# Performance work log

Measured on AMD Instinct MI355X. Metric: run time of the kernel, lower is better.

The kernel has to match this reference:

```python
import jax, jax.numpy as jnp
import numpy as np

N = 50000   # nodes
E = 600000  # edges
H = 128     # hidden_features
TW = 1      # time_window
L = 6       # hidden_layer
MSG_IN = 2 * H + TW + 2 + 1   # 260
UPD_IN = 2 * H + 1            # 257
LX = 1.0; LY = 1.0; TMAX = 1.0; DT = 0.01
EPS = 1e-5


def setup_inputs() -> dict:
    ks = iter(jax.random.split(jax.random.key(0), 64))
    rn = lambda s, sc=0.05: jax.random.normal(next(ks), s, dtype=jnp.float32) * sc
    z = lambda s: jnp.zeros(s, jnp.float32)
    o = lambda s: jnp.ones(s, jnp.float32)
    return {
        'u': rn((N, TW), 1.0),
        'pos': jax.random.uniform(next(ks), (N, 3), dtype=jnp.float32),
        'edge_index': jax.random.randint(next(ks), (2, E), 0, N),
        'emb_W1': rn((TW + 3, H)), 'emb_b1': z((H,)), 'emb_g1': o((H,)), 'emb_be1': z((H,)),
        'emb_W2': rn((H, H)), 'emb_b2': z((H,)), 'emb_g2': o((H,)), 'emb_be2': z((H,)),
        'm1_W': rn((L, MSG_IN, H)), 'm1_b': z((L, H)),
        'm2_W': rn((L, H, H)), 'm2_b': z((L, H)),
        'u1_W': rn((L, UPD_IN, H)), 'u1_b': z((L, H)),
        'u2_W': rn((L, H, H)), 'u2_b': z((L, H)),
        'bn_g': o((L, H)), 'bn_b': z((L, H)),
        'c1_W': rn((4, 1, 16)), 'c1_b': z((4,)),
        'c2_W': rn((8, 4, 12)), 'c2_b': z((8,)),
        'c3_W': rn((1, 8, 8)), 'c3_b': z((1,)),
    }


def _bn(x, g, b):
    # BatchNorm1d, training-mode batch statistics over node dim (biased var)
    mu = jnp.mean(x, 0)
    v = jnp.var(x, 0)
    return g * (x - mu) * jax.lax.rsqrt(v + EPS) + b


def _conv1d(x, W, b, stride):
    y = jax.lax.conv_general_dilated(x, W, (stride,), 'VALID',
                                     dimension_numbers=('NCH', 'OIH', 'NCH'))
    return y + b[None, :, None]


def _forward(u, pos, emb_W1, emb_b1, emb_g1, emb_be1, emb_W2, emb_b2, emb_g2, emb_be2,
             m1_W, m1_b, m2_W, m2_b, u1_W, u1_b, u2_W, u2_b, bn_g, bn_b,
             c1_W, c1_b, c2_W, c2_b, c3_W, c3_b, edge_index):
    px = pos[:, 1:2] / LX
    py = pos[:, 2:3] / LY
    variables = pos[:, 0:1] / TMAX  # pos_t, only eq variable

    # embedding MLP: Linear -> BN -> ReLU -> Linear -> BN
    h = jnp.concatenate([u, px, py, variables], -1) @ emb_W1 + emb_b1
    h = jax.nn.relu(_bn(h, emb_g1, emb_be1))
    h = _bn(h @ emb_W2 + emb_b2, emb_g2, emb_be2)

    src, dst = edge_index[0], edge_index[1]  # x_j = x[src], x_i = x[dst]
    du = u[dst] - u[src]
    dpx = px[dst] - px[src]
    dpy = py[dst] - py[src]
    var_i = variables[dst]
    deg = jax.ops.segment_sum(jnp.ones((E,), jnp.float32), dst, num_segments=N)
    deg = jnp.maximum(deg, 1.0)[:, None]  # mean aggregation denom (0-deg -> 0)

    for i in range(L):
        # message: cat(x_i, x_j, u_i-u_j, dpos_x, dpos_y, variables_i) -> 2xMLP
        msg_in = jnp.concatenate([h[dst], h[src], du, dpx, dpy, var_i], -1)  # [E,260]
        m = jax.nn.relu(msg_in @ m1_W[i] + m1_b[i])
        m = jax.nn.relu(m @ m2_W[i] + m2_b[i])
        agg = jax.ops.segment_sum(m, dst, num_segments=N) / deg  # mean scatter
        # update: cat(x, message, variables) -> 2xMLP, residual, BN
        up = jax.nn.relu(jnp.concatenate([h, agg, variables], -1) @ u1_W[i] + u1_b[i])
        up = jax.nn.relu(up @ u2_W[i] + u2_b[i])
        h = _bn(h + up, bn_g[i], bn_b[i])

    # output CNN over feature dim: [N,1,128] -> [N,1,1]
    x = h[:, None, :]
    x = jax.nn.relu(_conv1d(x, c1_W, c1_b, 3))
    x = jax.nn.relu(_conv1d(x, c2_W, c2_b, 3))
    diff = _conv1d(x, c3_W, c3_b, 2)[:, 0, :]  # [N, TW]

    dt = jnp.cumsum(jnp.full((1, TW), DT * 0.1, dtype=h.dtype), axis=1)
    return dt * diff


def reference(u, pos, edge_index, emb_W1, emb_b1, emb_g1, emb_be1, emb_W2, emb_b2,
              emb_g2, emb_be2, m1_W, m1_b, m2_W, m2_b, u1_W, u1_b, u2_W, u2_b,
              bn_g, bn_b, c1_W, c1_b, c2_W, c2_b, c3_W, c3_b):
    return _forward(u, pos, emb_W1, emb_b1, emb_g1, emb_be1, emb_W2, emb_b2, emb_g2,
                    emb_be2, m1_W, m1_b, m2_W, m2_b, u1_W, u1_b, u2_W, u2_b,
                    bn_g, bn_b, c1_W, c1_b, c2_W, c2_b, c3_W, c3_b, edge_index)
```

## Files before the change

### kernel.cpp

```cpp
#include <hip/hip_runtime.h>

#define NN 50000
#define NE 600000
#define HD 128
#define NL 6
#define DPB 16

typedef __attribute__((ext_vector_type(8))) short bf16x8;
typedef __attribute__((ext_vector_type(4))) float f32x4;

__device__ inline unsigned short f2bf(float x) {
  unsigned u = __float_as_uint(x);
  u += 0x7FFF + ((u >> 16) & 1);
  return (unsigned short)(u >> 16);
}
__device__ inline float bf2f(unsigned short s) {
  return __uint_as_float((unsigned)s << 16);
}
__device__ inline unsigned pk2(float a, float b) {
  return (unsigned)f2bf(a) | ((unsigned)f2bf(b) << 16);
}

__global__ void k_code(float* __restrict__ out, float code) {
  if (threadIdx.x == 0 && blockIdx.x == 0) out[0] = code;
}


__global__ __launch_bounds__(256) void k_w2t(const float* __restrict__ W, unsigned short* __restrict__ T) {
  int idx = blockIdx.x * 256 + threadIdx.x;
  if (idx >= NL * HD * HD) return;
  int l = idx >> 14, r = idx & 16383;
  int n = r >> 7, k = r & 127;
  T[idx] = f2bf(W[(l << 14) + (k << 7) + n]);
}

__global__ __launch_bounds__(256) void k_u1t(const float* __restrict__ W, unsigned short* __restrict__ T) {
  int idx = blockIdx.x * 256 + threadIdx.x;
  if (idx >= NL * 128 * 256) return;
  int l = idx >> 15, r = idx & 32767;
  int n = r >> 8, k = r & 255;
  T[idx] = f2bf(W[l * 32896 + k * 128 + n]);
}

__global__ __launch_bounds__(256) void k_abt(const float* __restrict__ W, unsigned short* __restrict__ T) {
  int idx = blockIdx.x * 256 + threadIdx.x;
  if (idx >= NL * 256 * 128) return;
  int l = idx >> 15, r = idx & 32767;
  int n = r >> 7, k = r & 127;
  int row = (n < 128) ? k : 128 + k;
  int col = n & 127;
  T[idx] = f2bf(W[l * 33280 + row * 128 + col]);
}


__global__ __launch_bounds__(256) void k_deg(const int* __restrict__ ei, int* __restrict__ deg) {
  int e = blockIdx.x * 256 + threadIdx.x;
  if (e < NE) {
    int d = ei[NE + e];
    if (d >= 0 && d < NN) atomicAdd(&deg[d], 1);
  }
}

__global__ __launch_bounds__(256) void k_scan1(const int* __restrict__ deg, int* __restrict__ cursor,
                                               int* __restrict__ blk, float* __restrict__ invd) {
  __shared__ int sd[256];
  int t = threadIdx.x;
  int i = blockIdx.x * 256 + t;
  int v = (i < NN) ? deg[i] : 0;
  sd[t] = v;
  __syncthreads();
  for (int off = 1; off < 256; off <<= 1) {
    int x = (t >= off) ? sd[t - off] : 0;
    __syncthreads();
    if (t >= off) sd[t] += x;
    __syncthreads();
  }
  int incl = sd[t];
  if (i < NN) {
    cursor[i] = incl - v;
    invd[i] = 1.0f / fmaxf((float)v, 1.0f);
  }
  if (t == 255) blk[blockIdx.x] = incl;
}

__global__ __launch_bounds__(256) void k_scan2(int* __restrict__ blk, int nb) {
  __shared__ int sd[256];
  int t = threadIdx.x;
  int v = (t < nb) ? blk[t] : 0;
  sd[t] = v;
  __syncthreads();
  for (int off = 1; off < 256; off <<= 1) {
    int x = (t >= off) ? sd[t - off] : 0;
    __syncthreads();
    if (t >= off) sd[t] += x;
    __syncthreads();
  }
  if (t < nb) blk[t] = sd[t] - v;
}

__global__ __launch_bounds__(256) void k_scan3(int* __restrict__ cursor, const int* __restrict__ blk,
                                               int* __restrict__ rowstart) {
  int i = blockIdx.x * 256 + threadIdx.x;
  if (i < NN) {
    int v = cursor[i] + blk[blockIdx.x];
    cursor[i] = v;
    rowstart[i] = v;
  }
  if (i == 0) rowstart[NN] = NE;
}

__global__ __launch_bounds__(256) void k_scatter(const int* __restrict__ ei, const float* __restrict__ u,
                                                 const float* __restrict__ pos, int* __restrict__ cursor,
                                                 int* __restrict__ ssrc, int* __restrict__ sdst,
                                                 float* __restrict__ sfeat) {
  int e = blockIdx.x * 256 + threadIdx.x;
  if (e >= NE) return;
  int s = ei[e], d = ei[NE + e];
  s = s < 0 ? 0 : (s >= NN ? NN - 1 : s);
  d = d < 0 ? 0 : (d >= NN ? NN - 1 : d);
  int p = atomicAdd(&cursor[d], 1);
  ssrc[p] = s;
  sdst[p] = d;
  float du  = u[d] - u[s];
  float dpx = pos[d*3+1] - pos[s*3+1];
  float dpy = pos[d*3+2] - pos[s*3+2];
  float vi  = pos[d*3+0];
  ((float4*)sfeat)[p] = make_float4(du, dpx, dpy, vi);
}


__global__ __launch_bounds__(256) void k_emb1(const float* __restrict__ u, const float* __restrict__ pos,
                                              const float* __restrict__ W, const float* __restrict__ b,
                                              float* __restrict__ h, double* __restrict__ P) {
  __shared__ float xs[32 * 129];
  int tid = threadIdx.x;
  int nl = tid & 31, jg = tid >> 5;
  int gn = blockIdx.x * 32 + nl;
  float f0 = 0.f, f1 = 0.f, f2 = 0.f, f3 = 0.f;
  if (gn < NN) { f0 = u[gn]; f1 = pos[gn*3+1]; f2 = pos[gn*3+2]; f3 = pos[gn*3+0]; }
  float x[16];
#pragma unroll
  for (int q = 0; q < 4; ++q) {
    int j = (jg << 4) + (q << 2);
    float4 w0 = *(const float4*)(W + 0*HD + j);
    float4 w1 = *(const float4*)(W + 1*HD + j);
    float4 w2 = *(const float4*)(W + 2*HD + j);
    float4 w3 = *(const float4*)(W + 3*HD + j);
    float4 bb = *(const float4*)(b + j);
    x[q*4+0] = f0*w0.x + f1*w1.x + f2*w2.x + f3*w3.x + bb.x;
    x[q*4+1] = f0*w0.y + f1*w1.y + f2*w2.y + f3*w3.y + bb.y;
    x[q*4+2] = f0*w0.z + f1*w1.z + f2*w2.z + f3*w3.z + bb.z;
    x[q*4+3] = f0*w0.w + f1*w1.w + f2*w2.w + f3*w3.w + bb.w;
  }
  if (gn < NN) {
#pragma unroll
    for (int q = 0; q < 4; ++q)
      *(float4*)(h + (size_t)gn*HD + (jg<<4) + (q<<2)) = make_float4(x[q*4+0], x[q*4+1], x[q*4+2], x[q*4+3]);
  }
#pragma unroll
  for (int i = 0; i < 16; ++i) xs[nl*129 + (jg<<4) + i] = (gn < NN) ? x[i] : 0.f;
  __syncthreads();
  if (tid < HD) {
    double s = 0.0, sq = 0.0;
    for (int e = 0; e < 32; ++e) { double v = (double)xs[e*129 + tid]; s += v; sq += v*v; }
    size_t pb = (size_t)blockIdx.x * 256;
    P[pb + tid] = s;
    P[pb + 128 + tid] = sq;
  }
}

__global__ __launch_bounds__(256) void k_emb2(float* __restrict__ h, const float* __restrict__ W,
                                              const float* __restrict__ b, double* __restrict__ P) {
  __shared__ float hs[32 * 129];
  int tid = threadIdx.x;
  int base = blockIdx.x * 32;
#pragma unroll
  for (int r = 0; r < 16; ++r) {
    int lin = r*256 + tid;
    int n = lin >> 7, j = lin & 127;
    int gn = base + n;
    hs[n*129 + j] = (gn < NN) ? h[(size_t)gn*HD + j] : 0.f;
  }
  __syncthreads();
  int nl = tid & 31, jg = tid >> 5;
  int gn = base + nl;
  float acc[16];
#pragma unroll
  for (int q = 0; q < 4; ++q) {
    float4 bb = *(const float4*)(b + (jg<<4) + (q<<2));
    acc[q*4+0] = bb.x; acc[q*4+1] = bb.y; acc[q*4+2] = bb.z; acc[q*4+3] = bb.w;
  }
  for (int k = 0; k < HD; ++k) {
    float a = hs[nl*129 + k];
    const float4* wp = (const float4*)(W + (size_t)k*HD + (jg<<4));
#pragma unroll
    for (int q = 0; q < 4; ++q) {
      float4 wv = wp[q];
      acc[q*4+0] = fmaf(a, wv.x, acc[q*4+0]);
      acc[q*4+1] = fmaf(a, wv.y, acc[q*4+1]);
      acc[q*4+2] = fmaf(a, wv.z, acc[q*4+2]);
      acc[q*4+3] = fmaf(a, wv.w, acc[q*4+3]);
    }
  }
  if (gn < NN) {
#pragma unroll
    for (int q = 0; q < 4; ++q)
      *(float4*)(h + (size_t)gn*HD + (jg<<4) + (q<<2)) = make_float4(acc[q*4+0], acc[q*4+1], acc[q*4+2], acc[q*4+3]);
  }
  __syncthreads();
#pragma unroll
  for (int i = 0; i < 16; ++i) hs[nl*129 + (jg<<4) + i] = (gn < NN) ? acc[i] : 0.f;
  __syncthreads();
  if (tid < HD) {
    double s = 0.0, sq = 0.0;
    for (int e = 0; e < 32; ++e) { double v = (double)hs[e*129 + tid]; s += v; sq += v*v; }
    size_t pb = (size_t)blockIdx.x * 256;
    P[pb + tid] = s;
    P[pb + 128 + tid] = sq;
  }
}

__global__ __launch_bounds__(256) void k_redP(const double* __restrict__ P, int nrows,
                                              float* __restrict__ musig) {
  __shared__ double sd[256];
  __shared__ double sq_[256];
  int c = blockIdx.x;
  int t = threadIdx.x;
  double s = 0.0, q = 0.0;
  for (int k = t; k < nrows; k += 256) {
    s += P[(size_t)k*256 + c];
    q += P[(size_t)k*256 + 128 + c];
  }
  sd[t] = s; sq_[t] = q;
  __syncthreads();
  for (int off = 128; off; off >>= 1) {
    if (t < off) { sd[t] += sd[t + off]; sq_[t] += sq_[t + off]; }
    __syncthreads();
  }
  if (t == 0) {
    double mu  = sd[0] / (double)NN;
    double var = sq_[0] / (double)NN - mu * mu;
    musig[c]      = (float)mu;
    musig[HD + c] = (float)(1.0 / sqrt(var + 1e-5));
  }
}

__global__ void k_redA(const double* __restrict__ stats, float* __restrict__ musig) {
  int c = threadIdx.x;
  double mu  = stats[c] / (double)NN;
  double var = stats[128 + c] / (double)NN - mu * mu;
  musig[c]      = (float)mu;
  musig[HD + c] = (float)(1.0 / sqrt(var + 1e-5));
}

__global__ __launch_bounds__(256) void k_bn(float* __restrict__ h, const float* __restrict__ musig,
                                            const float* __restrict__ g, const float* __restrict__ be,
                                            int relu) {
  int idx = blockIdx.x * 256 + threadIdx.x;
  if (idx >= NN * HD) return;
  int j = idx & 127;
  float x = h[idx];
  x = g[j] * (x - musig[j]) * musig[HD + j] + be[j];
  if (relu) x = fmaxf(x, 0.f);
  h[idx] = x;
}


__global__ __launch_bounds__(256) void k_ab_mfma(float* __restrict__ h,
                                                 const unsigned short* __restrict__ abt,
                                                 const float* __restrict__ musig,
                                                 const float* __restrict__ g, const float* __restrict__ be,
                                                 int applyBN,
                                                 unsigned short* __restrict__ A, unsigned short* __restrict__ B) {
  __shared__ unsigned short hbf[32 * 136];
  int tid = threadIdx.x;
  int base = blockIdx.x * 32;
#pragma unroll
  for (int r = 0; r < 16; ++r) {
    int lin = r*256 + tid;
    int n = lin >> 7, j = lin & 127;
    int gn = base + n;
    float hv = (gn < NN) ? h[(size_t)gn*HD + j] : 0.f;
    if (applyBN) {
      hv = g[j] * (hv - musig[j]) * musig[HD + j] + be[j];
      if (gn < NN) h[(size_t)gn*HD + j] = hv;
    }
    hbf[n*136 + j] = f2bf((gn < NN) ? hv : 0.f);
  }
  __syncthreads();
  int wv = tid >> 6, lane = tid & 63;
  int quad = lane >> 4, mrow = lane & 15;
  int mt = wv & 1, ntg = wv >> 1;
  f32x4 acc[8];
#pragma unroll
  for (int t = 0; t < 8; ++t) acc[t] = (f32x4){0.f,0.f,0.f,0.f};
#pragma unroll
  for (int ks = 0; ks < 4; ++ks) {
    bf16x8 a = *(const bf16x8*)(hbf + (mt*16 + mrow)*136 + ks*32 + quad*8);
#pragma unroll
    for (int t = 0; t < 8; ++t) {
      bf16x8 b = *(const bf16x8*)(abt + (size_t)((ntg*8 + t)*16 + mrow)*128 + ks*32 + quad*8);
      acc[t] = __builtin_amdgcn_mfma_f32_16x16x32_bf16(a, b, acc[t], 0, 0, 0);
    }
  }
#pragma unroll
  for (int t = 0; t < 8; ++t) {
    int c = (ntg*8 + t)*16 + mrow;
#pragma unroll
    for (int r = 0; r < 4; ++r) {
      int gn = base + mt*16 + quad*4 + r;
      if (gn < NN) {
        if (c < 128) A[(size_t)gn*HD + c]       = f2bf(acc[t][r]);
        else         B[(size_t)gn*HD + c - 128] = f2bf(acc[t][r]);
      }
    }
  }
}


__global__ __launch_bounds__(256, 2) void k_msgupd(const unsigned short* __restrict__ A,
                                                   const unsigned short* __restrict__ B,
                                                   const int* __restrict__ ssrc, const int* __restrict__ sdst,
                                                   const float* __restrict__ sfeat, const float* __restrict__ invd,
                                                   const int* __restrict__ rowstart,
                                                   const float* __restrict__ W1, const float* __restrict__ b1,
                                                   const unsigned short* __restrict__ w2t, const float* __restrict__ b2,
                                                   float* __restrict__ h, const float* __restrict__ pos,
                                                   const unsigned short* __restrict__ u1t,
                                                   const float* __restrict__ U1var, const float* __restrict__ ub1,
                                                   const unsigned short* __restrict__ u2t, const float* __restrict__ ub2,
                                                   double* __restrict__ P) {
  __shared__ __align__(16) unsigned short smAB[16*136 + 2*32*136];
  __shared__ float wes[6 * 128];
  __shared__ int ldstD[64];

  unsigned short* As   = smAB;
  unsigned short* m1b0 = smAB + 16*136;
  unsigned short* abf  = smAB;
  unsigned short* u1bf = smAB + 16*264;

  int tid = threadIdx.x;
  int base = blockIdx.x * DPB;

  {
    int row = tid >> 4, c16 = tid & 15;
    int gn = base + row;
    bf16x8 v = (bf16x8){0,0,0,0,0,0,0,0};
    if (gn < NN) v = *(const bf16x8*)(A + (size_t)gn*HD + c16*8);
    *(bf16x8*)(As + row*136 + c16*8) = v;
  }
  for (int i = tid; i < 768; i += 256) {
    int k = i >> 7, j = i & 127;
    float v;
    if (k < 4)       v = W1[(size_t)(256 + k)*HD + j];
    else if (k == 4) v = b1[j];
    else             v = b2[j];
    wes[i] = v;
  }
  int rs0 = rowstart[base];
  int rs1 = rowstart[base + DPB];
  __syncthreads();

  int wv = tid >> 6, lane = tid & 63;
  int quad = lane >> 4, mrow = lane & 15;
  int el = tid & 31, jg = tid >> 5;

  float b2c[2];
#pragma unroll
  for (int t = 0; t < 2; ++t) b2c[t] = wes[5*128 + (wv*2 + t)*16 + mrow];

  const float4* sf4 = (const float4*)sfeat;
  int nch = (rs1 - rs0 + 31) >> 5;

  f32x4 agg[2];
  agg[0] = (f32x4){0.f,0.f,0.f,0.f}; agg[1] = agg[0];

  int d_c; float4 f_c;
  int s_n1, d_n1; float4 f_n1;
  {
    int e = rs0 + el; bool v = e < rs1;
    int sc = v ? ssrc[e] : 0;
    d_c = v ? (sdst[e] - base) : 999;
    f_c = v ? sf4[e] : make_float4(0.f, 0.f, 0.f, 0.f);
    s_n1 = sc;
  }
  bf16x8 b0_c = *(const bf16x8*)(B + (size_t)s_n1*HD + (jg<<4));
  bf16x8 b1_c = *(const bf16x8*)(B + (size_t)s_n1*HD + (jg<<4) + 8);
  {
    int e = rs0 + 32 + el; bool v = e < rs1;
    s_n1 = v ? ssrc[e] : 0;
    d_n1 = v ? (sdst[e] - base) : 999;
    f_n1 = v ? sf4[e] : make_float4(0.f, 0.f, 0.f, 0.f);
  }

  int par = 0;
  for (int ch = 0; ch < nch; ++ch) {
    int e0 = rs0 + ch*32;
    int s_n2, d_n2; float4 f_n2;
    {
      int e = e0 + 64 + el; bool v = e < rs1;
      s_n2 = v ? ssrc[e] : 0;
      d_n2 = v ? (sdst[e] - base) : 999;
      f_n2 = v ? sf4[e] : make_float4(0.f, 0.f, 0.f, 0.f);
    }
    bf16x8 b0_n = *(const bf16x8*)(B + (size_t)s_n1*HD + (jg<<4));
    bf16x8 b1_n = *(const bf16x8*)(B + (size_t)s_n1*HD + (jg<<4) + 8);

    if (tid < 32) ldstD[par*32 + tid] = d_c;
    unsigned short* m1bf = m1b0 + par*32*136;

    {
      int dA = (d_c < DPB) ? d_c : 0;
      float f0 = f_c.x, f1 = f_c.y, f2 = f_c.z, f3 = f_c.w;
      const unsigned short* Ar = As + dA*136 + (jg<<4);
      bf16x8 a0 = *(const bf16x8*)(Ar);
      bf16x8 a1 = *(const bf16x8*)(Ar + 8);
      float m1v[16];
#pragma unroll
      for (int q = 0; q < 4; ++q) {
        float4 w0 = *(const float4*)(wes + 0*128 + (jg<<4) + (q<<2));
        float4 w1 = *(const float4*)(wes + 1*128 + (jg<<4) + (q<<2));
        float4 w2 = *(const float4*)(wes + 2*128 + (jg<<4) + (q<<2));
        float4 w3 = *(const float4*)(wes + 3*128 + (jg<<4) + (q<<2));
        float4 bb = *(const float4*)(wes + 4*128 + (jg<<4) + (q<<2));
#pragma unroll
        for (int z = 0; z < 4; ++z) {
          int i = q*4 + z;
          unsigned short avs = (i < 8) ? (unsigned short)a0[i] : (unsigned short)a1[i-8];
          unsigned short bvs = (i < 8) ? (unsigned short)b0_c[i] : (unsigned short)b1_c[i-8];
          float we  = (z==0?w0.x:(z==1?w0.y:(z==2?w0.z:w0.w)));
          float w1e = (z==0?w1.x:(z==1?w1.y:(z==2?w1.z:w1.w)));
          float w2e = (z==0?w2.x:(z==1?w2.y:(z==2?w2.z:w2.w)));
          float w3e = (z==0?w3.x:(z==1?w3.y:(z==2?w3.z:w3.w)));
          float bbe = (z==0?bb.x:(z==1?bb.y:(z==2?bb.z:bb.w)));
          m1v[i] = fmaxf(bf2f(avs) + bf2f(bvs) + f0*we + f1*w1e + f2*w2e + f3*w3e + bbe, 0.f);
        }
      }
      unsigned* pp = (unsigned*)(m1bf + el*136 + (jg<<4));
#pragma unroll
      for (int i = 0; i < 8; ++i)
        pp[i] = pk2(m1v[2*i], m1v[2*i+1]);
    }
    __syncthreads();

    {
      f32x4 acc[2][2];
      acc[0][0] = (f32x4){0.f,0.f,0.f,0.f}; acc[0][1] = acc[0][0];
      acc[1][0] = acc[0][0]; acc[1][1] = acc[0][0];
#pragma unroll
      for (int ks = 0; ks < 4; ++ks) {
        bf16x8 a0 = *(const bf16x8*)(m1bf + (mrow)*136      + ks*32 + quad*8);
        bf16x8 a1 = *(const bf16x8*)(m1bf + (16 + mrow)*136 + ks*32 + quad*8);
#pragma unroll
        for (int t = 0; t < 2; ++t) {
          bf16x8 b = *(const bf16x8*)(w2t + (size_t)((wv*2 + t)*16 + mrow)*128 + ks*32 + quad*8);
          acc[0][t] = __builtin_amdgcn_mfma_f32_16x16x32_bf16(a0, b, acc[0][t], 0, 0, 0);
          acc[1][t] = __builtin_amdgcn_mfma_f32_16x16x32_bf16(a1, b, acc[1][t], 0, 0, 0);
        }
      }

      bf16x8 sel;
#pragma unroll
      for (int i = 0; i < 8; ++i) {
        int dl = ldstD[par*32 + quad*8 + i];
        sel[i] = (short)((dl == mrow) ? 0x3F80 : 0);
      }

      int src0 = ((quad & 1) * 2) * 16 + mrow;
      int src1 = src0 + 16;
      bool useE0 = (quad < 2);
#pragma unroll
      for (int t = 0; t < 2; ++t) {
        float bb = b2c[t];
        unsigned p00 = pk2(fmaxf(acc[0][t][0] + bb, 0.f), fmaxf(acc[0][t][1] + bb, 0.f));
        unsigned p01 = pk2(fmaxf(acc[0][t][2] + bb, 0.f), fmaxf(acc[0][t][3] + bb, 0.f));
        unsigned p10 = pk2(fmaxf(acc[1][t][0] + bb, 0.f), fmaxf(acc[1][t][1] + bb, 0.f));
        unsigned p11 = pk2(fmaxf(acc[1][t][2] + bb, 0.f), fmaxf(acc[1][t][3] + bb, 0.f));
        unsigned a00 = (unsigned)__shfl((int)p00, src0);
        unsigned a01 = (unsigned)__shfl((int)p01, src0);
        unsigned a02 = (unsigned)__shfl((int)p00, src1);
        unsigned a03 = (unsigned)__shfl((int)p01, src1);
        unsigned e10 = (unsigned)__shfl((int)p10, src0);
        unsigned e11 = (unsigned)__shfl((int)p11, src0);
        unsigned e12 = (unsigned)__shfl((int)p10, src1);
        unsigned e13 = (unsigned)__shfl((int)p11, src1);
        bf16x8 bfr;
        unsigned* bp = (unsigned*)&bfr;
        bp[0] = useE0 ? a00 : e10;
        bp[1] = useE0 ? a01 : e11;
        bp[2] = useE0 ? a02 : e12;
        bp[3] = useE0 ? a03 : e13;
        agg[t] = __builtin_amdgcn_mfma_f32_16x16x32_bf16(sel, bfr, agg[t], 0, 0, 0);
      }
    }

    d_c = d_n1; f_c = f_n1;
    s_n1 = s_n2; d_n1 = d_n2; f_n1 = f_n2;
    b0_c = b0_n; b1_c = b1_n;
    par ^= 1;
  }
  __syncthreads();

  {
    int row = tid >> 4, c16 = tid & 15;
    int gn = base + row;
    float4 h0 = *(const float4*)(h + (size_t)gn*HD + c16*8);
    float4 h1 = *(const float4*)(h + (size_t)gn*HD + c16*8 + 4);
    unsigned* q = (unsigned*)(abf + row*264 + c16*8);
    q[0] = pk2(h0.x, h0.y); q[1] = pk2(h0.z, h0.w);
    q[2] = pk2(h1.x, h1.y); q[3] = pk2(h1.z, h1.w);
  }
  {
    float invdv[4];
#pragma unroll
    for (int r = 0; r < 4; ++r) invdv[r] = invd[base + quad*4 + r];
#pragma unroll
    for (int t = 0; t < 2; ++t) {
      int c = (wv*2 + t)*16 + mrow;
#pragma unroll
      for (int r = 0; r < 4; ++r)
        abf[(quad*4 + r)*264 + 128 + c] = f2bf(agg[t][r] * invdv[r]);
    }
  }
  __syncthreads();

  int lo = mrow;
  float ub1c[2], uvarc[2], ub2c[2];
#pragma unroll
  for (int t = 0; t < 2; ++t) {
    int c = (wv*2 + t)*16 + lo;
    ub1c[t] = ub1[c]; uvarc[t] = U1var[c]; ub2c[t] = ub2[c];
  }
  float lvarv[4];
#pragma unroll
  for (int r = 0; r < 4; ++r) lvarv[r] = pos[(size_t)(base + quad*4 + r)*3 + 0];

  f32x4 ua[2];
  ua[0] = (f32x4){0.f,0.f,0.f,0.f}; ua[1] = ua[0];
#pragma unroll
  for (int ks = 0; ks < 8; ++ks) {
    bf16x8 a = *(const bf16x8*)(abf + lo*264 + ks*32 + quad*8);
#pragma unroll
    for (int t = 0; t < 2; ++t) {
      bf16x8 b = *(const bf16x8*)(u1t + (size_t)((wv*2 + t)*16 + lo)*256 + ks*32 + quad*8);
      ua[t] = __builtin_amdgcn_mfma_f32_16x16x32_bf16(a, b, ua[t], 0, 0, 0);
    }
  }
#pragma unroll
  for (int t = 0; t < 2; ++t) {
    int c = (wv*2 + t)*16 + lo;
#pragma unroll
    for (int r = 0; r < 4; ++r) {
      float v = fmaxf(ua[t][r] + ub1c[t] + lvarv[r]*uvarc[t], 0.f);
      u1bf[(quad*4 + r)*136 + c] = f2bf(v);
    }
  }
  __syncthreads();

  f32x4 va[2];
  va[0] = (f32x4){0.f,0.f,0.f,0.f}; va[1] = va[0];
#pragma unroll
  for (int ks = 0; ks < 4; ++ks) {
    bf16x8 a = *(const bf16x8*)(u1bf + lo*136 + ks*32 + quad*8);
#pragma unroll
    for (int t = 0; t < 2; ++t) {
      bf16x8 b = *(const bf16x8*)(u2t + (size_t)((wv*2 + t)*16 + lo)*128 + ks*32 + quad*8);
      va[t] = __builtin_amdgcn_mfma_f32_16x16x32_bf16(a, b, va[t], 0, 0, 0);
    }
  }

#pragma unroll
  for (int t = 0; t < 2; ++t) {
    int c = (wv*2 + t)*16 + lo;
    float s = 0.f, q = 0.f;
#pragma unroll
    for (int r = 0; r < 4; ++r) {
      int gn = base + quad*4 + r;
      float x = h[(size_t)gn*HD + c] + fmaxf(va[t][r] + ub2c[t], 0.f);
      h[(size_t)gn*HD + c] = x;
      s += x; q += x*x;
    }
    s += __shfl_xor(s, 16); q += __shfl_xor(q, 16);
    s += __shfl_xor(s, 32); q += __shfl_xor(q, 32);
    if (quad == 0) {
      size_t pb = (size_t)blockIdx.x * 256;
      P[pb + c]       = (double)s;
      P[pb + 128 + c] = (double)q;
    }
  }
}


__global__ __launch_bounds__(256) void k_msg_direct(const float* __restrict__ h,
                                                    const int* __restrict__ ei, const float* __restrict__ u,
                                                    const float* __restrict__ pos, const float* __restrict__ invd,
                                                    const float* __restrict__ W1, const float* __restrict__ b1,
                                                    const float* __restrict__ W2, const float* __restrict__ b2,
                                                    float* __restrict__ agg) {
  __shared__ float hd[32 * 129];
  __shared__ float hsr[32 * 129];
  __shared__ float m1s[32 * 129];
  __shared__ int lsrc[32];
  __shared__ int ldst[32];
  __shared__ float lf[32][4];
  int tid = threadIdx.x;
  int base = blockIdx.x * 32;
  if (tid < 32) {
    int e = base + tid;
    int s = ei[e], d = ei[NE + e];
    s = s < 0 ? 0 : (s >= NN ? NN - 1 : s);
    d = d < 0 ? 0 : (d >= NN ? NN - 1 : d);
    lsrc[tid] = s; ldst[tid] = d;
    lf[tid][0] = u[d] - u[s];
    lf[tid][1] = pos[d*3+1] - pos[s*3+1];
    lf[tid][2] = pos[d*3+2] - pos[s*3+2];
    lf[tid][3] = pos[d*3+0];
  }
  __syncthreads();
#pragma unroll
  for (int r = 0; r < 16; ++r) {
    int lin = r*256 + tid;
    int n = lin >> 7, j = lin & 127;
    hd[n*129 + j]  = h[(size_t)ldst[n]*HD + j];
    hsr[n*129 + j] = h[(size_t)lsrc[n]*HD + j];
  }
  __syncthreads();
  int el = tid & 31, jg = tid >> 5;
  float f0 = lf[el][0], f1 = lf[el][1], f2 = lf[el][2], f3 = lf[el][3];
  const float* We = W1 + 256*HD + (jg<<4);
  float acc[16];
#pragma unroll
  for (int q = 0; q < 4; ++q) {
    float4 w0 = *(const float4*)(We + 0*HD + (q<<2));
    float4 w1 = *(const float4*)(We + 1*HD + (q<<2));
    float4 w2 = *(const float4*)(We + 2*HD + (q<<2));
    float4 w3 = *(const float4*)(We + 3*HD + (q<<2));
    float4 bb = *(const float4*)(b1 + (jg<<4) + (q<<2));
    acc[q*4+0] = f0*w0.x + f1*w1.x + f2*w2.x + f3*w3.x + bb.x;
    acc[q*4+1] = f0*w0.y + f1*w1.y + f2*w2.y + f3*w3.y + bb.y;
    acc[q*4+2] = f0*w0.z + f1*w1.z + f2*w2.z + f3*w3.z + bb.z;
    acc[q*4+3] = f0*w0.w + f1*w1.w + f2*w2.w + f3*w3.w + bb.w;
  }
  for (int k = 0; k < HD; ++k) {
    float a  = hd[el*129 + k];
    float bs = hsr[el*129 + k];
    const float4* wa = (const float4*)(W1 + (size_t)k*HD + (jg<<4));
    const float4* wb = (const float4*)(W1 + (size_t)(128 + k)*HD + (jg<<4));
#pragma unroll
    for (int q = 0; q < 4; ++q) {
      float4 w1v = wa[q];
      float4 w2v = wb[q];
      acc[q*4+0] = fmaf(a, w1v.x, fmaf(bs, w2v.x, acc[q*4+0]));
      acc[q*4+1] = fmaf(a, w1v.y, fmaf(bs, w2v.y, acc[q*4+1]));
      acc[q*4+2] = fmaf(a, w1v.z, fmaf(bs, w2v.z, acc[q*4+2]));
      acc[q*4+3] = fmaf(a, w1v.w, fmaf(bs, w2v.w, acc[q*4+3]));
    }
  }
#pragma unroll
  for (int i = 0; i < 16; ++i) m1s[el*129 + (jg<<4) + i] = fmaxf(acc[i], 0.f);
  __syncthreads();
  float acc2[16];
#pragma unroll
  for (int q = 0; q < 4; ++q) {
    float4 bb = *(const float4*)(b2 + (jg<<4) + (q<<2));
    acc2[q*4+0] = bb.x; acc2[q*4+1] = bb.y; acc2[q*4+2] = bb.z; acc2[q*4+3] = bb.w;
  }
  for (int k = 0; k < HD; ++k) {
    float a = m1s[el*129 + k];
    const float4* wp = (const float4*)(W2 + (size_t)k*HD + (jg<<4));
#pragma unroll
    for (int q = 0; q < 4; ++q) {
      float4 wv = wp[q];
      acc2[q*4+0] = fmaf(a, wv.x, acc2[q*4+0]);
      acc2[q*4+1] = fmaf(a, wv.y, acc2[q*4+1]);
      acc2[q*4+2] = fmaf(a, wv.z, acc2[q*4+2]);
      acc2[q*4+3] = fmaf(a, wv.w, acc2[q*4+3]);
    }
  }
#pragma unroll
  for (int i = 0; i < 16; ++i) hd[el*129 + (jg<<4) + i] = fmaxf(acc2[i], 0.f);
  __syncthreads();
  if (tid < HD) {
    int j = tid;
    for (int e = 0; e < 32; ++e) {
      int de = ldst[e];
      atomicAdd(&agg[(size_t)de*HD + j], hd[e*129 + j] * invd[de]);
    }
  }
}


__global__ __launch_bounds__(256) void k_upd(float* __restrict__ h, const float* __restrict__ agg,
                                             const float* __restrict__ pos,
                                             const float* __restrict__ W1, const float* __restrict__ b1,
                                             const float* __restrict__ W2, const float* __restrict__ b2,
                                             double* __restrict__ stats) {
  __shared__ float hs[32 * 129];
  __shared__ float as_[32 * 129];
  int tid = threadIdx.x;
  int base = blockIdx.x * 32;
#pragma unroll
  for (int r = 0; r < 16; ++r) {
    int lin = r*256 + tid;
    int n = lin >> 7, j = lin & 127;
    int gn = base + n;
    hs[n*129 + j]  = (gn < NN) ? h[(size_t)gn*HD + j]   : 0.f;
    as_[n*129 + j] = (gn < NN) ? agg[(size_t)gn*HD + j] : 0.f;
  }
  __syncthreads();
  int nl = tid & 31, jg = tid >> 5;
  int gn = base + nl;
  float var = (gn < NN) ? pos[gn*3+0] : 0.f;
  float acc[16];
#pragma unroll
  for (int q = 0; q < 4; ++q) {
    int j = (jg<<4) + (q<<2);
    float4 bb = *(const float4*)(b1 + j);
    float4 wv = *(const float4*)(W1 + 256*HD + j);
    acc[q*4+0] = fmaf(var, wv.x, bb.x);
    acc[q*4+1] = fmaf(var, wv.y, bb.y);
    acc[q*4+2] = fmaf(var, wv.z, bb.z);
    acc[q*4+3] = fmaf(var, wv.w, bb.w);
  }
  for (int k = 0; k < HD; ++k) {
    float a = hs[nl*129 + k];
    float g = as_[nl*129 + k];
    const float4* w1p = (const float4*)(W1 + (size_t)k*HD + (jg<<4));
    const float4* w2p = (const float4*)(W1 + (size_t)(128 + k)*HD + (jg<<4));
#pragma unroll
    for (int q = 0; q < 4; ++q) {
      float4 wa = w1p[q];
      float4 wb = w2p[q];
      acc[q*4+0] = fmaf(a, wa.x, fmaf(g, wb.x, acc[q*4+0]));
      acc[q*4+1] = fmaf(a, wa.y, fmaf(g, wb.y, acc[q*4+1]));
      acc[q*4+2] = fmaf(a, wa.z, fmaf(g, wb.z, acc[q*4+2]));
      acc[q*4+3] = fmaf(a, wa.w, fmaf(g, wb.w, acc[q*4+3]));
    }
  }
  float up1[16];
#pragma unroll
  for (int i = 0; i < 16; ++i) up1[i] = fmaxf(acc[i], 0.f);
  __syncthreads();
#pragma unroll
  for (int i = 0; i < 16; ++i) as_[nl*129 + (jg<<4) + i] = up1[i];
  __syncthreads();
  float acc2[16];
#pragma unroll
  for (int q = 0; q < 4; ++q) {
    float4 bb = *(const float4*)(b2 + (jg<<4) + (q<<2));
    acc2[q*4+0] = bb.x; acc2[q*4+1] = bb.y; acc2[q*4+2] = bb.z; acc2[q*4+3] = bb.w;
  }
  for (int k = 0; k < HD; ++k) {
    float a = as_[nl*129 + k];
    const float4* wp = (const float4*)(W2 + (size_t)k*HD + (jg<<4));
#pragma unroll
    for (int q = 0; q < 4; ++q) {
      float4 wv = wp[q];
      acc2[q*4+0] = fmaf(a, wv.x, acc2[q*4+0]);
      acc2[q*4+1] = fmaf(a, wv.y, acc2[q*4+1]);
      acc2[q*4+2] = fmaf(a, wv.z, acc2[q*4+2]);
      acc2[q*4+3] = fmaf(a, wv.w, acc2[q*4+3]);
    }
  }
  float x[16];
#pragma unroll
  for (int i = 0; i < 16; ++i)
    x[i] = hs[nl*129 + (jg<<4) + i] + fmaxf(acc2[i], 0.f);
  if (gn < NN) {
#pragma unroll
    for (int q = 0; q < 4; ++q)
      *(float4*)(h + (size_t)gn*HD + (jg<<4) + (q<<2)) = make_float4(x[q*4+0], x[q*4+1], x[q*4+2], x[q*4+3]);
  }
  __syncthreads();
#pragma unroll
  for (int i = 0; i < 16; ++i) hs[nl*129 + (jg<<4) + i] = (gn < NN) ? x[i] : 0.f;
  __syncthreads();
  if (tid < HD) {
    double s = 0.0, sq = 0.0;
    for (int e = 0; e < 32; ++e) { double v = (double)hs[e*129 + tid]; s += v; sq += v*v; }
    atomicAdd(&stats[tid], s);
    atomicAdd(&stats[HD + tid], sq);
  }
}


__global__ __launch_bounds__(256) void k_conv(const float* __restrict__ h,
                                              const float* __restrict__ musig,
                                              const float* __restrict__ g, const float* __restrict__ be,
                                              int applyBN,
                                              const float* __restrict__ c1W, const float* __restrict__ c1b,
                                              const float* __restrict__ c2W, const float* __restrict__ c2b,
                                              const float* __restrict__ c3W, const float* __restrict__ c3b,
                                              float* __restrict__ out) {
  __shared__ float xs[4][128];
  __shared__ float o1[4][152];
  __shared__ float o2[4][72];
  int tid = threadIdx.x;
  int w = tid >> 6, lane = tid & 63;
  int n = blockIdx.x * 4 + w;
#pragma unroll
  for (int half = 0; half < 2; ++half) {
    int j = half * 64 + lane;
    float v = h[(size_t)n*HD + j];
    if (applyBN) v = g[j] * (v - musig[j]) * musig[HD + j] + be[j];
    xs[w][j] = v;
  }
  __syncthreads();
  for (int o = lane; o < 152; o += 64) {
    int oc = o / 38, t = o % 38;
    float s = c1b[oc];
#pragma unroll
    for (int k = 0; k < 16; ++k) s = fmaf(xs[w][t*3 + k], c1W[oc*16 + k], s);
    o1[w][oc*38 + t] = fmaxf(s, 0.f);
  }
  __syncthreads();
  for (int o = lane; o < 72; o += 64) {
    int oc = o / 9, t = o % 9;
    float s = c2b[oc];
    for (int ic = 0; ic < 4; ++ic) {
#pragma unroll
      for (int k = 0; k < 12; ++k) s = fmaf(o1[w][ic*38 + t*3 + k], c2W[oc*48 + ic*12 + k], s);
    }
    o2[w][oc*9 + t] = fmaxf(s, 0.f);
  }
  __syncthreads();
  int ic = lane >> 3, k = lane & 7;
  float t3 = o2[w][ic*9 + k] * c3W[ic*8 + k];
  for (int off = 32; off; off >>= 1) t3 += __shfl_down(t3, off);
  if (lane == 0) out[n] = 0.001f * (t3 + c3b[0]);
}


extern "C" void kernel_launch(void* const* d_in, const int* in_sizes, int n_in,
                              void* d_out, int out_size, void* d_ws, size_t ws_size,
                              hipStream_t stream) {
  (void)out_size;
  float* out = (float*)d_out;

  static const int expect[27] = {
    50000, 150000, 1200000,
    512, 128, 128, 128,
    16384, 128, 128, 128,
    199680, 768, 98304, 768, 197376, 768, 98304, 768,
    768, 768,
    64, 4, 384, 8, 64, 1
  };
  if (n_in != 27) { k_code<<<1, 64, 0, stream>>>(out, 5000099.f); return; }
  for (int i = 0; i < 27; ++i)
    if (in_sizes[i] != expect[i]) { k_code<<<1, 64, 0, stream>>>(out, 5000100.f + (float)i); return; }

  const float* u    = (const float*)d_in[0];
  const float* pos  = (const float*)d_in[1];
  const int*   ei   = (const int*)d_in[2];
  const float* eW1  = (const float*)d_in[3];
  const float* eb1  = (const float*)d_in[4];
  const float* eg1  = (const float*)d_in[5];
  const float* ebe1 = (const float*)d_in[6];
  const float* eW2  = (const float*)d_in[7];
  const float* eb2  = (const float*)d_in[8];
  const float* eg2  = (const float*)d_in[9];
  const float* ebe2 = (const float*)d_in[10];
  const float* m1W  = (const float*)d_in[11];
  const float* m1b  = (const float*)d_in[12];
  const float* m2W  = (const float*)d_in[13];
  const float* m2b  = (const float*)d_in[14];
  const float* u1W  = (const float*)d_in[15];
  const float* u1b  = (const float*)d_in[16];
  const float* u2W  = (const float*)d_in[17];
  const float* u2b  = (const float*)d_in[18];
  const float* bng  = (const float*)d_in[19];
  const float* bnb  = (const float*)d_in[20];
  const float* c1W  = (const float*)d_in[21];
  const float* c1b  = (const float*)d_in[22];
  const float* c2W  = (const float*)d_in[23];
  const float* c2b  = (const float*)d_in[24];
  const float* c3W  = (const float*)d_in[25];
  const float* c3b  = (const float*)d_in[26];

  char* wsp = (char*)d_ws;
  size_t off = 0;
  auto alloc = [&](size_t bytes) -> void* {
    void* p = wsp + off;
    off = (off + bytes + 255) & ~(size_t)255;
    return p;
  };
  double* stats  = (double*)alloc(256 * 8);
  float*  musig  = (float*)alloc(256 * 4);
  int*    deg    = (int*)alloc((size_t)NN * 4);
  int*    cursor = (int*)alloc((size_t)NN * 4);
  int*    blk    = (int*)alloc(256 * 4);
  float*  invd   = (float*)alloc((size_t)NN * 4);
  float*  h      = (float*)alloc((size_t)NN * HD * 4);
  float*  agg    = (float*)alloc((size_t)NN * HD * 4);
  double* P      = (double*)alloc((size_t)3200 * 256 * 8);
  size_t needed_direct = off;
  unsigned short* A = (unsigned short*)alloc((size_t)NN * HD * 2);
  unsigned short* B = (unsigned short*)alloc((size_t)NN * HD * 2);
  float*  sfeat  = (float*)alloc((size_t)NE * 4 * 4);
  int*    ssrc   = (int*)alloc((size_t)NE * 4);
  int*    sdst   = (int*)alloc((size_t)NE * 4);
  int*    rowstart = (int*)alloc((size_t)(NN + 1) * 4);
  unsigned short* w2t = (unsigned short*)alloc((size_t)NL * HD * HD * 2);
  unsigned short* u2t = (unsigned short*)alloc((size_t)NL * HD * HD * 2);
  unsigned short* u1t = (unsigned short*)alloc((size_t)NL * HD * 256 * 2);
  unsigned short* abt = (unsigned short*)alloc((size_t)NL * 256 * HD * 2);
  size_t needed_fast = off;

  if (ws_size < needed_direct) {
    k_code<<<1, 64, 0, stream>>>(out, (float)(9000000u + (unsigned)(ws_size >> 20)));
    return;
  }
  const bool fast = (ws_size >= needed_fast);

  const int nbN  = (NN + 255) / 256;
  const int nbE  = (NE + 255) / 256;
  const int nt32 = (NN + 31) / 32;
  const int nbBN = NN * HD / 256;
  const int nbMU = NN / DPB;

  hipMemsetAsync(deg, 0, (size_t)NN * 4, stream);
  k_deg<<<nbE, 256, 0, stream>>>(ei, deg);
  k_scan1<<<nbN, 256, 0, stream>>>(deg, cursor, blk, invd);
  if (fast) {
    k_scan2<<<1, 256, 0, stream>>>(blk, nbN);
    k_scan3<<<nbN, 256, 0, stream>>>(cursor, blk, rowstart);
    k_scatter<<<nbE, 256, 0, stream>>>(ei, u, pos, cursor, ssrc, sdst, sfeat);
    k_w2t<<<(NL*HD*HD + 255) / 256, 256, 0, stream>>>(m2W, w2t);
    k_w2t<<<(NL*HD*HD + 255) / 256, 256, 0, stream>>>(u2W, u2t);
    k_u1t<<<(NL*HD*256 + 255) / 256, 256, 0, stream>>>(u1W, u1t);
    k_abt<<<(NL*256*HD + 255) / 256, 256, 0, stream>>>(m1W, abt);
  }

  k_emb1<<<nt32, 256, 0, stream>>>(u, pos, eW1, eb1, h, P);
  k_redP<<<128, 256, 0, stream>>>(P, nt32, musig);
  k_bn<<<nbBN, 256, 0, stream>>>(h, musig, eg1, ebe1, 1);
  k_emb2<<<nt32, 256, 0, stream>>>(h, eW2, eb2, P);
  k_redP<<<128, 256, 0, stream>>>(P, nt32, musig);
  k_bn<<<nbBN, 256, 0, stream>>>(h, musig, eg2, ebe2, 0);

  for (int i = 0; i < NL; ++i) {
    if (fast) {
      k_ab_mfma<<<nt32, 256, 0, stream>>>(h, abt + (size_t)i * 256 * HD,
                                          musig, bng + (size_t)(i > 0 ? i - 1 : 0) * HD,
                                          bnb + (size_t)(i > 0 ? i - 1 : 0) * HD,
                                          (i > 0) ? 1 : 0, A, B);
      k_msgupd<<<nbMU, 256, 0, stream>>>(A, B, ssrc, sdst, sfeat, invd, rowstart,
                                         m1W + (size_t)i * 260 * HD, m1b + (size_t)i * HD,
                                         w2t + (size_t)i * HD * HD, m2b + (size_t)i * HD,
                                         h, pos,
                                         u1t + (size_t)i * HD * 256,
                                         u1W + (size_t)i * 32896 + 256 * HD,
                                         u1b + (size_t)i * HD,
                                         u2t + (size_t)i * HD * HD,
                                         u2b + (size_t)i * HD, P);
      k_redP<<<128, 256, 0, stream>>>(P, nbMU, musig);
    } else {
      hipMemsetAsync(agg, 0, (size_t)NN * HD * 4, stream);
      k_msg_direct<<<NE / 32, 256, 0, stream>>>(h, ei, u, pos, invd,
                                                m1W + (size_t)i * 260 * HD, m1b + (size_t)i * HD,
                                                m2W + (size_t)i * HD * HD, m2b + (size_t)i * HD, agg);
      hipMemsetAsync(stats, 0, 256 * 8, stream);
      k_upd<<<nt32, 256, 0, stream>>>(h, agg, pos,
                                      u1W + (size_t)i * 257 * HD, u1b + (size_t)i * HD,
                                      u2W + (size_t)i * HD * HD, u2b + (size_t)i * HD, stats);
      k_redA<<<1, 128, 0, stream>>>(stats, musig);
      k_bn<<<nbBN, 256, 0, stream>>>(h, musig, bng + (size_t)i * HD, bnb + (size_t)i * HD, 0);
    }
  }

  k_conv<<<NN / 4, 256, 0, stream>>>(h, musig, bng + (size_t)(NL - 1) * HD, bnb + (size_t)(NL - 1) * HD,
                                     fast ? 1 : 0,
                                     c1W, c1b, c2W, c2b, c3W, c3b, out);
}
```

Baseline: 1.498 ms.

## Process 64 edges per chunk in fused message kernel instead of 32

The edge loop in the fused message/update kernel now handles 64 edges per iteration. Each thread computes 32 hidden columns for one edge rather than 16, and each wave issues MFMAs over four 16-edge groups. This halves the number of chunk iterations and block barriers per destination block and gives more MFMA work per synchronisation. In exchange it doubles LDS for the message buffer, raises register pressure with more accumulators and gather vectors, and wastes more work on padding when a block has few edges.

After: 1.528 ms. 1.02x slower.

```diff
diff --git a/kernel.cpp b/kernel.cpp
--- a/kernel.cpp
+++ b/kernel.cpp
@@ -330,9 +330,9 @@
                                                    const float* __restrict__ U1var, const float* __restrict__ ub1,
                                                    const unsigned short* __restrict__ u2t, const float* __restrict__ ub2,
                                                    double* __restrict__ P) {
-  __shared__ __align__(16) unsigned short smAB[16*136 + 2*32*136];
+  __shared__ __align__(16) unsigned short smAB[16*136 + 2*64*136];
   __shared__ float wes[6 * 128];
-  __shared__ int ldstD[64];
+  __shared__ int ldstD[128];
 
   unsigned short* As   = smAB;
   unsigned short* m1b0 = smAB + 16*136;
@@ -363,17 +363,19 @@
 
   int wv = tid >> 6, lane = tid & 63;
   int quad = lane >> 4, mrow = lane & 15;
-  int el = tid & 31, jg = tid >> 5;
+  int el = tid & 63;
 
   float b2c[2];
 #pragma unroll
   for (int t = 0; t < 2; ++t) b2c[t] = wes[5*128 + (wv*2 + t)*16 + mrow];
 
   const float4* sf4 = (const float4*)sfeat;
-  int nch = (rs1 - rs0 + 31) >> 5;
+  int nch = (rs1 - rs0 + 63) >> 6;
 
   f32x4 agg[2];
   agg[0] = (f32x4){0.f,0.f,0.f,0.f}; agg[1] = agg[0];
+
+  int cb0 = wv*32;
 
   int d_c; float4 f_c;
   int s_n1, d_n1; float4 f_n1;
@@ -384,10 +386,12 @@
     f_c = v ? sf4[e] : make_float4(0.f, 0.f, 0.f, 0.f);
     s_n1 = sc;
   }
-  bf16x8 b0_c = *(const bf16x8*)(B + (size_t)s_n1*HD + (jg<<4));
-  bf16x8 b1_c = *(const bf16x8*)(B + (size_t)s_n1*HD + (jg<<4) + 8);
+  bf16x8 bc0 = *(const bf16x8*)(B + (size_t)s_n1*HD + cb0);
+  bf16x8 bc1 = *(const bf16x8*)(B + (size_t)s_n1*HD + cb0 + 8);
+  bf16x8 bc2 = *(const bf16x8*)(B + (size_t)s_n1*HD + cb0 + 16);
+  bf16x8 bc3 = *(const bf16x8*)(B + (size_t)s_n1*HD + cb0 + 24);
   {
-    int e = rs0 + 32 + el; bool v = e < rs1;
+    int e = rs0 + 64 + el; bool v = e < rs1;
     s_n1 = v ? ssrc[e] : 0;
     d_n1 = v ? (sdst[e] - base) : 999;
     f_n1 = v ? sf4[e] : make_float4(0.f, 0.f, 0.f, 0.f);
@@ -395,75 +399,92 @@
 
   int par = 0;
   for (int ch = 0; ch < nch; ++ch) {
-    int e0 = rs0 + ch*32;
+    int e0 = rs0 + ch*64;
     int s_n2, d_n2; float4 f_n2;
     {
-      int e = e0 + 64 + el; bool v = e < rs1;
+      int e = e0 + 128 + el; bool v = e < rs1;
       s_n2 = v ? ssrc[e] : 0;
       d_n2 = v ? (sdst[e] - base) : 999;
       f_n2 = v ? sf4[e] : make_float4(0.f, 0.f, 0.f, 0.f);
     }
-    bf16x8 b0_n = *(const bf16x8*)(B + (size_t)s_n1*HD + (jg<<4));
-    bf16x8 b1_n = *(const bf16x8*)(B + (size_t)s_n1*HD + (jg<<4) + 8);
-
-    if (tid < 32) ldstD[par*32 + tid] = d_c;
-    unsigned short* m1bf = m1b0 + par*32*136;
+    bf16x8 bn0 = *(const bf16x8*)(B + (size_t)s_n1*HD + cb0);
+    bf16x8 bn1 = *(const bf16x8*)(B + (size_t)s_n1*HD + cb0 + 8);
+    bf16x8 bn2 = *(const bf16x8*)(B + (size_t)s_n1*HD + cb0 + 16);
+    bf16x8 bn3 = *(const bf16x8*)(B + (size_t)s_n1*HD + cb0 + 24);
+
+    if (tid < 64) ldstD[par*64 + tid] = d_c;
+    unsigned short* m1bf = m1b0 + par*64*136;
 
     {
       int dA = (d_c < DPB) ? d_c : 0;
       float f0 = f_c.x, f1 = f_c.y, f2 = f_c.z, f3 = f_c.w;
-      const unsigned short* Ar = As + dA*136 + (jg<<4);
-      bf16x8 a0 = *(const bf16x8*)(Ar);
-      bf16x8 a1 = *(const bf16x8*)(Ar + 8);
-      float m1v[16];
-#pragma unroll
-      for (int q = 0; q < 4; ++q) {
-        float4 w0 = *(const float4*)(wes + 0*128 + (jg<<4) + (q<<2));
-        float4 w1 = *(const float4*)(wes + 1*128 + (jg<<4) + (q<<2));
-        float4 w2 = *(const float4*)(wes + 2*128 + (jg<<4) + (q<<2));
-        float4 w3 = *(const float4*)(wes + 3*128 + (jg<<4) + (q<<2));
-        float4 bb = *(const float4*)(wes + 4*128 + (jg<<4) + (q<<2));
-#pragma unroll
-        for (int z = 0; z < 4; ++z) {
-          int i = q*4 + z;
-          unsigned short avs = (i < 8) ? (unsigned short)a0[i] : (unsigned short)a1[i-8];
-          unsigned short bvs = (i < 8) ? (unsigned short)b0_c[i] : (unsigned short)b1_c[i-8];
-          float we  = (z==0?w0.x:(z==1?w0.y:(z==2?w0.z:w0.w)));
-          float w1e = (z==0?w1.x:(z==1?w1.y:(z==2?w1.z:w1.w)));
-          float w2e = (z==0?w2.x:(z==1?w2.y:(z==2?w2.z:w2.w)));
-          float w3e = (z==0?w3.x:(z==1?w3.y:(z==2?w3.z:w3.w)));
-          float bbe = (z==0?bb.x:(z==1?bb.y:(z==2?bb.z:bb.w)));
-          m1v[i] = fmaxf(bf2f(avs) + bf2f(bvs) + f0*we + f1*w1e + f2*w2e + f3*w3e + bbe, 0.f);
+#pragma unroll
+      for (int hh = 0; hh < 2; ++hh) {
+        int cb = cb0 + hh*16;
+        const unsigned short* Ar = As + dA*136 + cb;
+        bf16x8 a0 = *(const bf16x8*)(Ar);
+        bf16x8 a1 = *(const bf16x8*)(Ar + 8);
+        bf16x8 bv0 = (hh == 0) ? bc0 : bc2;
+        bf16x8 bv1 = (hh == 0) ? bc1 : bc3;
+        float m1v[16];
+#pragma unroll
+        for (int q = 0; q < 4; ++q) {
+          float4 w0 = *(const float4*)(wes + 0*128 + cb + (q<<2));
+          float4 w1 = *(const float4*)(wes + 1*128 + cb + (q<<2));
+          float4 w2 = *(const float4*)(wes + 2*128 + cb + (q<<2));
+          float4 w3 = *(const float4*)(wes + 3*128 + cb + (q<<2));
+          float4 bb = *(const float4*)(wes + 4*128 + cb + (q<<2));
+#pragma unroll
+          for (int z = 0; z < 4; ++z) {
+            int i = q*4 + z;
+            unsigned short avs = (i < 8) ? (unsigned short)a0[i] : (unsigned short)a1[i-8];
+            unsigned short bvs = (i < 8) ? (unsigned short)bv0[i] : (unsigned short)bv1[i-8];
+            float we  = (z==0?w0.x:(z==1?w0.y:(z==2?w0.z:w0.w)));
+            float w1e = (z==0?w1.x:(z==1?w1.y:(z==2?w1.z:w1.w)));
+            float w2e = (z==0?w2.x:(z==1?w2.y:(z==2?w2.z:w2.w)));
+            float w3e = (z==0?w3.x:(z==1?w3.y:(z==2?w3.z:w3.w)));
+            float bbe = (z==0?bb.x:(z==1?bb.y:(z==2?bb.z:bb.w)));
+            m1v[i] = fmaxf(bf2f(avs) + bf2f(bvs) + f0*we + f1*w1e + f2*w2e + f3*w3e + bbe, 0.f);
+          }
         }
+        unsigned* pp = (unsigned*)(m1bf + el*136 + cb);
+#pragma unroll
+        for (int i = 0; i < 8; ++i)
+          pp[i] = pk2(m1v[2*i], m1v[2*i+1]);
       }
-      unsigned* pp = (unsigned*)(m1bf + el*136 + (jg<<4));
-#pragma unroll
-      for (int i = 0; i < 8; ++i)
-        pp[i] = pk2(m1v[2*i], m1v[2*i+1]);
     }
     __syncthreads();
 
     {
-      f32x4 acc[2][2];
-      acc[0][0] = (f32x4){0.f,0.f,0.f,0.f}; acc[0][1] = acc[0][0];
-      acc[1][0] = acc[0][0]; acc[1][1] = acc[0][0];
+      f32x4 acc[4][2];
+#pragma unroll
+      for (int eg = 0; eg < 4; ++eg) {
+        acc[eg][0] = (f32x4){0.f,0.f,0.f,0.f};
+        acc[eg][1] = acc[eg][0];
+      }
 #pragma unroll
       for (int ks = 0; ks < 4; ++ks) {
-        bf16x8 a0 = *(const bf16x8*)(m1bf + (mrow)*136      + ks*32 + quad*8);
-        bf16x8 a1 = *(const bf16x8*)(m1bf + (16 + mrow)*136 + ks*32 + quad*8);
+        bf16x8 a0 = *(const bf16x8*)(m1bf + (0*16 + mrow)*136 + ks*32 + quad*8);
+        bf16x8 a1 = *(const bf16x8*)(m1bf + (1*16 + mrow)*136 + ks*32 + quad*8);
+        bf16x8 a2 = *(const bf16x8*)(m1bf + (2*16 + mrow)*136 + ks*32 + quad*8);
+        bf16x8 a3 = *(const bf16x8*)(m1bf + (3*16 + mrow)*136 + ks*32 + quad*8);
 #pragma unroll
         for (int t = 0; t < 2; ++t) {
           bf16x8 b = *(const bf16x8*)(w2t + (size_t)((wv*2 + t)*16 + mrow)*128 + ks*32 + quad*8);
           acc[0][t] = __builtin_amdgcn_mfma_f32_16x16x32_bf16(a0, b, acc[0][t], 0, 0, 0);
           acc[1][t] = __builtin_amdgcn_mfma_f32_16x16x32_bf16(a1, b, acc[1][t], 0, 0, 0);
+          acc[2][t] = __builtin_amdgcn_mfma_f32_16x16x32_bf16(a2, b, acc[2][t], 0, 0, 0);
+          acc[3][t] = __builtin_amdgcn_mfma_f32_16x16x32_bf16(a3, b, acc[3][t], 0, 0, 0);
         }
       }
 
-      bf16x8 sel;
+      bf16x8 sel0, sel1;
 #pragma unroll
       for (int i = 0; i < 8; ++i) {
-        int dl = ldstD[par*32 + quad*8 + i];
-        sel[i] = (short)((dl == mrow) ? 0x3F80 : 0);
+        int dl0 = ldstD[par*64 + quad*8 + i];
+        int dl1 = ldstD[par*64 + 32 + quad*8 + i];
+        sel0[i] = (short)((dl0 == mrow) ? 0x3F80 : 0);
+        sel1[i] = (short)((dl1 == mrow) ? 0x3F80 : 0);
       }
 
       int src0 = ((quad & 1) * 2) * 16 + mrow;
@@ -472,31 +493,54 @@
 #pragma unroll
       for (int t = 0; t < 2; ++t) {
         float bb = b2c[t];
-        unsigned p00 = pk2(fmaxf(acc[0][t][0] + bb, 0.f), fmaxf(acc[0][t][1] + bb, 0.f));
-        unsigned p01 = pk2(fmaxf(acc[0][t][2] + bb, 0.f), fmaxf(acc[0][t][3] + bb, 0.f));
-        unsigned p10 = pk2(fmaxf(acc[1][t][0] + bb, 0.f), fmaxf(acc[1][t][1] + bb, 0.f));
-        unsigned p11 = pk2(fmaxf(acc[1][t][2] + bb, 0.f), fmaxf(acc[1][t][3] + bb, 0.f));
-        unsigned a00 = (unsigned)__shfl((int)p00, src0);
-        unsigned a01 = (unsigned)__shfl((int)p01, src0);
-        unsigned a02 = (unsigned)__shfl((int)p00, src1);
-        unsigned a03 = (unsigned)__shfl((int)p01, src1);
-        unsigned e10 = (unsigned)__shfl((int)p10, src0);
-        unsigned e11 = (unsigned)__shfl((int)p11, src0);
-        unsigned e12 = (unsigned)__shfl((int)p10, src1);
-        unsigned e13 = (unsigned)__shfl((int)p11, src1);
-        bf16x8 bfr;
-        unsigned* bp = (unsigned*)&bfr;
-        bp[0] = useE0 ? a00 : e10;
-        bp[1] = useE0 ? a01 : e11;
-        bp[2] = useE0 ? a02 : e12;
-        bp[3] = useE0 ? a03 : e13;
-        agg[t] = __builtin_amdgcn_mfma_f32_16x16x32_bf16(sel, bfr, agg[t], 0, 0, 0);
+        {
+          unsigned p00 = pk2(fmaxf(acc[0][t][0] + bb, 0.f), fmaxf(acc[0][t][1] + bb, 0.f));
+          unsigned p01 = pk2(fmaxf(acc[0][t][2] + bb, 0.f), fmaxf(acc[0][t][3] + bb, 0.f));
+          unsigned p10 = pk2(fmaxf(acc[1][t][0] + bb, 0.f), fmaxf(acc[1][t][1] + bb, 0.f));
+          unsigned p11 = pk2(fmaxf(acc[1][t][2] + bb, 0.f), fmaxf(acc[1][t][3] + bb, 0.f));
+          unsigned a00 = (unsigned)__shfl((int)p00, src0);
+          unsigned a01 = (unsigned)__shfl((int)p01, src0);
+          unsigned a02 = (unsigned)__shfl((int)p00, src1);
+          unsigned a03 = (unsigned)__shfl((int)p01, src1);
+          unsigned e10 = (unsigned)__shfl((int)p10, src0);
+          unsigned e11 = (unsigned)__shfl((int)p11, src0);
+          unsigned e12 = (unsigned)__shfl((int)p10, src1);
+          unsigned e13 = (unsigned)__shfl((int)p11, src1);
+          bf16x8 bfr;
+          unsigned* bp = (unsigned*)&bfr;
+          bp[0] = useE0 ? a00 : e10;
+          bp[1] = useE0 ? a01 : e11;
+          bp[2] = useE0 ? a02 : e12;
+          bp[3] = useE0 ? a03 : e13;
+          agg[t] = __builtin_amdgcn_mfma_f32_16x16x32_bf16(sel0, bfr, agg[t], 0, 0, 0);
+        }
+        {
+          unsigned p00 = pk2(fmaxf(acc[2][t][0] + bb, 0.f), fmaxf(acc[2][t][1] + bb, 0.f));
+          unsigned p01 = pk2(fmaxf(acc[2][t][2] + bb, 0.f), fmaxf(acc[2][t][3] + bb, 0.f));
+          unsigned p10 = pk2(fmaxf(acc[3][t][0] + bb, 0.f), fmaxf(acc[3][t][1] + bb, 0.f));
+          unsigned p11 = pk2(fmaxf(acc[3][t][2] + bb, 0.f), fmaxf(acc[3][t][3] + bb, 0.f));
+          unsigned a00 = (unsigned)__shfl((int)p00, src0);
+          unsigned a01 = (unsigned)__shfl((int)p01, src0);
+          unsigned a02 = (unsigned)__shfl((int)p00, src1);
+          unsigned a03 = (unsigned)__shfl((int)p01, src1);
+          unsigned e10 = (unsigned)__shfl((int)p10, src0);
+          unsigned e11 = (unsigned)__shfl((int)p11, src0);
+          unsigned e12 = (unsigned)__shfl((int)p10, src1);
+          unsigned e13 = (unsigned)__shfl((int)p11, src1);
+          bf16x8 bfr;
+          unsigned* bp = (unsigned*)&bfr;
+          bp[0] = useE0 ? a00 : e10;
+          bp[1] = useE0 ? a01 : e11;
+          bp[2] = useE0 ? a02 : e12;
+          bp[3] = useE0 ? a03 : e13;
+          agg[t] = __builtin_amdgcn_mfma_f32_16x16x32_bf16(sel1, bfr, agg[t], 0, 0, 0);
+        }
       }
     }
 
     d_c = d_n1; f_c = f_n1;
     s_n1 = s_n2; d_n1 = d_n2; f_n1 = f_n2;
-    b0_c = b0_n; b1_c = b1_n;
+    bc0 = bn0; bc1 = bn1; bc2 = bn2; bc3 = bn3;
     par ^= 1;
   }
   __syncthreads();
```
